# Kernel tuning notes

Measured on AMD Instinct MI355X. Metric: run time of the kernel, lower is better.

## Reference

```python
import jax, jax.numpy as jnp
import numpy as np

E = 300000
N_ATOMS = 10000
C = 256
RBF = 16
NUM_TARGET = 1


def setup_inputs() -> dict:
    key = jax.random.key(0)
    ks = jax.random.split(key, 12)
    s = lambda fan_in: 1.0 / np.sqrt(fan_in)
    return {
        "x": jax.random.normal(ks[0], (E, C), dtype=jnp.float32),
        "rbf": jax.random.uniform(ks[1], (E, RBF), dtype=jnp.float32),
        "num_atoms": N_ATOMS,
        "edge_index_0": jax.random.randint(ks[2], (E,), 0, N_ATOMS, dtype=jnp.int64),
        # lin_rbf: Linear(rbf_dim -> in_channels)
        "w_rbf": jax.random.normal(ks[3], (C, RBF), dtype=jnp.float32) * s(RBF),
        "b_rbf": jnp.zeros((C,), dtype=jnp.float32),
        # mlp: Linear(C,C), SiLU, Linear(C,C), SiLU, Linear(C, num_target)
        "w1": jax.random.normal(ks[4], (C, C), dtype=jnp.float32) * s(C),
        "b1": jnp.zeros((C,), dtype=jnp.float32),
        "w2": jax.random.normal(ks[5], (C, C), dtype=jnp.float32) * s(C),
        "b2": jnp.zeros((C,), dtype=jnp.float32),
        "w3": jax.random.normal(ks[6], (NUM_TARGET, C), dtype=jnp.float32) * s(C),
        "b3": jnp.zeros((NUM_TARGET,), dtype=jnp.float32),
    }


def reference(x, rbf, num_atoms, edge_index_0, w_rbf, b_rbf, w1, b1, w2, b2, w3, b3):
    # rbf_filter = lin_rbf(rbf): [E, C]
    rbf_filter = rbf @ w_rbf.T + b_rbf
    msg = rbf_filter * x  # [E, C]
    # scatter_add over edge source -> per-atom features [num_atoms, C]
    out = jax.ops.segment_sum(msg, edge_index_0, num_segments=num_atoms)
    # MLP: Linear+SiLU, Linear+SiLU, Linear
    out = jax.nn.silu(out @ w1.T + b1)
    out = jax.nn.silu(out @ w2.T + b2)
    out = out @ w3.T + b3  # [num_atoms, num_target]
    return out
```

## Files before the change

kernel.cpp:

```cpp
#include <hip/hip_runtime.h>
#include <math.h>

#define CDIM 256
#define RBFD 16
#define NATOMS 10000

__device__ __forceinline__ float dot4f(float4 a, float4 b) {
  return a.x * b.x + a.y * b.y + a.z * b.z + a.w * b.w;
}

__global__ void hist_kernel(const int* __restrict__ eidx, int* __restrict__ counts,
                            int E) {
  const int i = blockIdx.x * blockDim.x + threadIdx.x;
  if (i < E) atomicAdd(&counts[eidx[i]], 1);
}

__global__ void scan_kernel(const int* __restrict__ counts,
                            int* __restrict__ offsets, int* __restrict__ cursor) {
  __shared__ int part[256];
  const int t = threadIdx.x;
  const int CH = (NATOMS + 255) / 256;
  const int base = t * CH;
  const int n = min(CH, max(0, NATOMS - base));
  int s = 0;
  for (int j = 0; j < n; ++j) s += counts[base + j];
  part[t] = s;
  __syncthreads();
  for (int off = 1; off < 256; off <<= 1) {
    int v = 0;
    if (t >= off) v = part[t - off];
    __syncthreads();
    part[t] += v;
    __syncthreads();
  }
  int run = part[t] - s;
  for (int j = 0; j < n; ++j) {
    offsets[base + j] = run;
    cursor[base + j] = run;
    run += counts[base + j];
  }
  if (t == 255) offsets[NATOMS] = part[255];
}

__global__ void scatter_kernel(const int* __restrict__ eidx,
                               int* __restrict__ cursor, int* __restrict__ elist,
                               int E) {
  const int i = blockIdx.x * blockDim.x + threadIdx.x;
  if (i < E) {
    const int a = eidx[i];
    const int pos = atomicAdd(&cursor[a], 1);
    elist[pos] = i;
  }
}

__global__ __launch_bounds__(256) void gather_kernel(
    const float* __restrict__ x, const float* __restrict__ rbf,
    const int* __restrict__ elist, const int* __restrict__ offsets,
    const float* __restrict__ w_rbf, const float* __restrict__ b_rbf,
    float* __restrict__ acc) {
  const int lane = threadIdx.x & 63;
  const int atom = (blockIdx.x * blockDim.x + threadIdx.x) >> 6;
  if (atom >= NATOMS) return;
  const int c0 = lane * 4;

  const int start = offsets[atom];
  const int end = offsets[atom + 1];

  float4 wv[4][4];
  const float4 bb = *(const float4*)(b_rbf + c0);
#pragma unroll
  for (int j = 0; j < 4; ++j) {
    const float4* wr = (const float4*)(w_rbf + (size_t)(c0 + j) * RBFD);
    wv[j][0] = wr[0];
    wv[j][1] = wr[1];
    wv[j][2] = wr[2];
    wv[j][3] = wr[3];
  }

  if (end <= start) {
    *(float4*)(acc + (size_t)atom * CDIM + c0) = make_float4(0.f, 0.f, 0.f, 0.f);
    return;
  }
  const int last = end - 1;

  float4 sumA = make_float4(0.f, 0.f, 0.f, 0.f);
  float4 sumB = make_float4(0.f, 0.f, 0.f, 0.f);
  float4 sumC = make_float4(0.f, 0.f, 0.f, 0.f);

  float4 xA, xB, xC;
  float4 rA0, rA1, rA2, rA3;
  float4 rB0, rB1, rB2, rB3;
  float4 rC0, rC1, rC2, rC3;

#define LOADD(S, idv)                                                        \
  {                                                                          \
    const int e_ = __builtin_amdgcn_readfirstlane(idv);                      \
    x##S = *(const float4*)(x + (size_t)e_ * CDIM + c0);                     \
    const float4* q_ = (const float4*)(rbf + (size_t)e_ * RBFD);             \
    r##S##0 = q_[0];                                                         \
    r##S##1 = q_[1];                                                         \
    r##S##2 = q_[2];                                                         \
    r##S##3 = q_[3];                                                         \
  }

#define COMPUTE(S, sum)                                                      \
  {                                                                          \
    float4 f_;                                                               \
    f_.x = bb.x + dot4f(wv[0][0], r##S##0) + dot4f(wv[0][1], r##S##1) +      \
           dot4f(wv[0][2], r##S##2) + dot4f(wv[0][3], r##S##3);              \
    f_.y = bb.y + dot4f(wv[1][0], r##S##0) + dot4f(wv[1][1], r##S##1) +      \
           dot4f(wv[1][2], r##S##2) + dot4f(wv[1][3], r##S##3);              \
    f_.z = bb.z + dot4f(wv[2][0], r##S##0) + dot4f(wv[2][1], r##S##1) +      \
           dot4f(wv[2][2], r##S##2) + dot4f(wv[2][3], r##S##3);              \
    f_.w = bb.w + dot4f(wv[3][0], r##S##0) + dot4f(wv[3][1], r##S##1) +      \
           dot4f(wv[3][2], r##S##2) + dot4f(wv[3][3], r##S##3);              \
    sum.x += f_.x * x##S.x;                                                  \
    sum.y += f_.y * x##S.y;                                                  \
    sum.z += f_.z * x##S.z;                                                  \
    sum.w += f_.w * x##S.w;                                                  \
  }

  int idA = elist[start];
  int idB = elist[min(start + 1, last)];
  int idC = elist[min(start + 2, last)];
  LOADD(A, idA)
  LOADD(B, idB)

  int i = start;
  for (; i + 3 <= end; i += 3) {
    idA = elist[min(i + 3, last)];
    LOADD(C, idC)
    COMPUTE(A, sumA)
    idB = elist[min(i + 4, last)];
    LOADD(A, idA)
    COMPUTE(B, sumB)
    idC = elist[min(i + 5, last)];
    LOADD(B, idB)
    COMPUTE(C, sumC)
  }
  const int k = end - i;
  if (k >= 1) COMPUTE(A, sumA)
  if (k >= 2) COMPUTE(B, sumB)

#undef LOADD
#undef COMPUTE

  float4 sum;
  sum.x = sumA.x + sumB.x + sumC.x;
  sum.y = sumA.y + sumB.y + sumC.y;
  sum.z = sumA.z + sumB.z + sumC.z;
  sum.w = sumA.w + sumB.w + sumC.w;
  *(float4*)(acc + (size_t)atom * CDIM + c0) = sum;
}

__global__ void transpose_kernel(const float* __restrict__ w1,
                                 const float* __restrict__ w2,
                                 float* __restrict__ w1T,
                                 float* __restrict__ w2T) {
  __shared__ float tile[32][33];
  const float* src = blockIdx.z ? w2 : w1;
  float* dst = blockIdx.z ? w2T : w1T;
  const int bx = blockIdx.x * 32;
  const int by = blockIdx.y * 32;
  const int tx = threadIdx.x, ty = threadIdx.y;
#pragma unroll
  for (int i = 0; i < 32; i += 8)
    tile[ty + i][tx] = src[(size_t)(by + ty + i) * CDIM + bx + tx];
  __syncthreads();
#pragma unroll
  for (int i = 0; i < 32; i += 8)
    dst[(size_t)(bx + ty + i) * CDIM + by + tx] = tile[tx][ty + i];
}

__global__ __launch_bounds__(256, 2) void mlp_kernel(
    const float* __restrict__ hin, const float* __restrict__ w1T,
    const float* __restrict__ b1, const float* __restrict__ w2T,
    const float* __restrict__ b2, const float* __restrict__ w3,
    const float* __restrict__ b3, float* __restrict__ out, int natoms) {
  __shared__ float H[32 * 256];
  __shared__ float WK[32 * 256];
  const int tid = threadIdx.x;
  const int tc = tid & 31;
  const int ta = tid >> 5;
  const int a0 = blockIdx.x * 32;
  const int cA = tc * 4;
  const int cB = 128 + tc * 4;

  {
    const float4* src = (const float4*)hin + (size_t)a0 * 64;
    float4* Hv = (float4*)H;
#pragma unroll
    for (int i = 0; i < 8; ++i) {
      const int idx = tid + i * 256;
      const int ga = a0 + (idx >> 6);
      Hv[idx] = (ga < natoms) ? src[idx] : make_float4(0.f, 0.f, 0.f, 0.f);
    }
  }

  float s[4][8];

#pragma unroll 1
  for (int layer = 0; layer < 2; ++layer) {
    const float* wT = (layer == 0) ? w1T : w2T;
    const float* bias = (layer == 0) ? b1 : b2;
    float r[4][8];
    const float4 bA = *(const float4*)(bias + cA);
    const float4 bB = *(const float4*)(bias + cB);
#pragma unroll
    for (int a = 0; a < 4; ++a) {
      r[a][0] = bA.x; r[a][1] = bA.y; r[a][2] = bA.z; r[a][3] = bA.w;
      r[a][4] = bB.x; r[a][5] = bB.y; r[a][6] = bB.z; r[a][7] = bB.w;
    }

    for (int k0 = 0; k0 < 256; k0 += 32) {
      __syncthreads();
      {
        const float4* wsrc = (const float4*)(wT + (size_t)k0 * CDIM);
        float4* WKv = (float4*)WK;
#pragma unroll
        for (int i = 0; i < 8; ++i) WKv[tid + i * 256] = wsrc[tid + i * 256];
      }
      __syncthreads();

#pragma unroll
      for (int kk = 0; kk < 32; kk += 4) {
        float4 ha[4];
#pragma unroll
        for (int a = 0; a < 4; ++a)
          ha[a] = *(const float4*)&H[(ta * 4 + a) * 256 + k0 + kk];
#pragma unroll
        for (int u = 0; u < 4; ++u) {
          const float4 w0 = *(const float4*)&WK[(kk + u) * 256 + cA];
          const float4 w1v = *(const float4*)&WK[(kk + u) * 256 + cB];
#pragma unroll
          for (int a = 0; a < 4; ++a) {
            const float hv = (u == 0) ? ha[a].x
                           : (u == 1) ? ha[a].y
                           : (u == 2) ? ha[a].z : ha[a].w;
            r[a][0] += hv * w0.x;  r[a][1] += hv * w0.y;
            r[a][2] += hv * w0.z;  r[a][3] += hv * w0.w;
            r[a][4] += hv * w1v.x; r[a][5] += hv * w1v.y;
            r[a][6] += hv * w1v.z; r[a][7] += hv * w1v.w;
          }
        }
      }
    }

#pragma unroll
    for (int a = 0; a < 4; ++a)
#pragma unroll
      for (int j = 0; j < 8; ++j) {
        const float v = r[a][j];
        s[a][j] = v / (1.0f + __expf(-v));
      }

    if (layer == 0) {
      __syncthreads();
#pragma unroll
      for (int a = 0; a < 4; ++a) {
        *(float4*)&H[(ta * 4 + a) * 256 + cA] =
            make_float4(s[a][0], s[a][1], s[a][2], s[a][3]);
        *(float4*)&H[(ta * 4 + a) * 256 + cB] =
            make_float4(s[a][4], s[a][5], s[a][6], s[a][7]);
      }
    }
  }

  const float4 w3a = *(const float4*)(w3 + cA);
  const float4 w3b = *(const float4*)(w3 + cB);
  float part[4];
#pragma unroll
  for (int a = 0; a < 4; ++a) {
    part[a] = s[a][0] * w3a.x + s[a][1] * w3a.y + s[a][2] * w3a.z +
              s[a][3] * w3a.w + s[a][4] * w3b.x + s[a][5] * w3b.y +
              s[a][6] * w3b.z + s[a][7] * w3b.w;
  }
  __syncthreads();
  float* red = WK;
#pragma unroll
  for (int a = 0; a < 4; ++a) red[(ta * 4 + a) * 33 + tc] = part[a];
  __syncthreads();
  if (tid < 32) {
    float sum = 0.f;
#pragma unroll
    for (int j = 0; j < 32; ++j) sum += red[tid * 33 + j];
    const int ga = a0 + tid;
    if (ga < natoms) out[ga] = sum + b3[0];
  }
}

extern "C" void kernel_launch(void* const* d_in, const int* in_sizes, int n_in,
                              void* d_out, int out_size, void* d_ws,
                              size_t ws_size, hipStream_t stream) {
  const float* x = (const float*)d_in[0];
  const float* rbf = (const float*)d_in[1];
  const int* eidx = (const int*)d_in[3];
  const float* w_rbf = (const float*)d_in[4];
  const float* b_rbf = (const float*)d_in[5];
  const float* w1 = (const float*)d_in[6];
  const float* b1 = (const float*)d_in[7];
  const float* w2 = (const float*)d_in[8];
  const float* b2 = (const float*)d_in[9];
  const float* w3 = (const float*)d_in[10];
  const float* b3 = (const float*)d_in[11];
  float* out = (float*)d_out;
  const int E = in_sizes[0] / CDIM;

  char* p = (char*)d_ws;
  float* acc = (float*)p;              p += (size_t)NATOMS * CDIM * sizeof(float);
  float* w1T = (float*)p;              p += CDIM * CDIM * sizeof(float);
  float* w2T = (float*)p;              p += CDIM * CDIM * sizeof(float);
  int* counts = (int*)p;               p += NATOMS * sizeof(int);
  int* offsets = (int*)p;              p += (NATOMS + 1) * sizeof(int);
  int* cursor = (int*)p;               p += NATOMS * sizeof(int);
  int* elist = (int*)p;                p += (size_t)E * sizeof(int);

  hipMemsetAsync(counts, 0, NATOMS * sizeof(int), stream);
  hist_kernel<<<(E + 255) / 256, 256, 0, stream>>>(eidx, counts, E);
  scan_kernel<<<1, 256, 0, stream>>>(counts, offsets, cursor);
  scatter_kernel<<<(E + 255) / 256, 256, 0, stream>>>(eidx, cursor, elist, E);
  transpose_kernel<<<dim3(8, 8, 2), dim3(32, 8), 0, stream>>>(w1, w2, w1T, w2T);
  gather_kernel<<<(NATOMS * 64 + 255) / 256, 256, 0, stream>>>(
      x, rbf, elist, offsets, w_rbf, b_rbf, acc);
  mlp_kernel<<<(NATOMS + 31) / 32, 256, 0, stream>>>(acc, w1T, b1, w2T, b2, w3,
                                                     b3, out, NATOMS);
}
```

Measured before the change: 629.9 us.

## Use one block per atom with one channel per thread in gather

The gather kernel now assigns a whole 256-thread block to each atom, with each thread owning a single channel, where before one wavefront per atom had each lane handle four channels. Each thread keeps only 16 filter weights in registers instead of 64, and launch bounds ask for 5 blocks per CU to raise occupancy and latency hiding. The cost is that four wavefronts now each re-read the same elist entries and rbf rows, and x is loaded as scalar floats rather than float4 vectors.

Measured after the change: 627.1 us. About the same (-0.5%).

```diff
diff --git a/kernel.cpp b/kernel.cpp
--- a/kernel.cpp
+++ b/kernel.cpp
@@ -5,7 +5,7 @@
 #define RBFD 16
 #define NATOMS 10000
 
-__device__ __forceinline__ float dot4f(float4 a, float4 b) {
+__device__ __forceinline__ float dot44(float4 a, float4 b) {
   return a.x * b.x + a.y * b.y + a.z * b.z + a.w * b.w;
 }
 
@@ -53,50 +53,47 @@
   }
 }
 
-__global__ __launch_bounds__(256) void gather_kernel(
+__global__ __launch_bounds__(256, 5) void gather_kernel(
     const float* __restrict__ x, const float* __restrict__ rbf,
     const int* __restrict__ elist, const int* __restrict__ offsets,
     const float* __restrict__ w_rbf, const float* __restrict__ b_rbf,
     float* __restrict__ acc) {
-  const int lane = threadIdx.x & 63;
-  const int atom = (blockIdx.x * blockDim.x + threadIdx.x) >> 6;
-  if (atom >= NATOMS) return;
-  const int c0 = lane * 4;
-
-  const int start = offsets[atom];
-  const int end = offsets[atom + 1];
-
-  float4 wv[4][4];
-  const float4 bb = *(const float4*)(b_rbf + c0);
-#pragma unroll
-  for (int j = 0; j < 4; ++j) {
-    const float4* wr = (const float4*)(w_rbf + (size_t)(c0 + j) * RBFD);
-    wv[j][0] = wr[0];
-    wv[j][1] = wr[1];
-    wv[j][2] = wr[2];
-    wv[j][3] = wr[3];
-  }
+  const int tid = threadIdx.x;
+  const int lane = tid & 63;
+  const int w = tid >> 6;
+  const int atom = blockIdx.x;
+  const int ch = w * 64 + lane;
+
+  const int start = __builtin_amdgcn_readfirstlane(offsets[atom]);
+  const int end = __builtin_amdgcn_readfirstlane(offsets[atom + 1]);
+
+  float4 wv0, wv1, wv2, wv3;
+  {
+    const float4* wr = (const float4*)(w_rbf + (size_t)ch * RBFD);
+    wv0 = wr[0];
+    wv1 = wr[1];
+    wv2 = wr[2];
+    wv3 = wr[3];
+  }
+  const float bb = b_rbf[ch];
 
   if (end <= start) {
-    *(float4*)(acc + (size_t)atom * CDIM + c0) = make_float4(0.f, 0.f, 0.f, 0.f);
+    acc[(size_t)atom * CDIM + ch] = 0.f;
     return;
   }
   const int last = end - 1;
 
-  float4 sumA = make_float4(0.f, 0.f, 0.f, 0.f);
-  float4 sumB = make_float4(0.f, 0.f, 0.f, 0.f);
-  float4 sumC = make_float4(0.f, 0.f, 0.f, 0.f);
-
-  float4 xA, xB, xC;
+  float sumA = 0.f, sumB = 0.f, sumC = 0.f;
+
+  float xA, xB, xC;
   float4 rA0, rA1, rA2, rA3;
   float4 rB0, rB1, rB2, rB3;
   float4 rC0, rC1, rC2, rC3;
 
-#define LOADD(S, idv)                                                        \
+#define LOADD(S, eid)                                                        \
   {                                                                          \
-    const int e_ = __builtin_amdgcn_readfirstlane(idv);                      \
-    x##S = *(const float4*)(x + (size_t)e_ * CDIM + c0);                     \
-    const float4* q_ = (const float4*)(rbf + (size_t)e_ * RBFD);             \
+    x##S = x[(size_t)(eid)*CDIM + ch];           \
+    const float4* q_ = (const float4*)(rbf + (size_t)(eid)*RBFD);            \
     r##S##0 = q_[0];                                                         \
     r##S##1 = q_[1];                                                         \
     r##S##2 = q_[2];                                                         \
@@ -105,36 +102,26 @@
 
 #define COMPUTE(S, sum)                                                      \
   {                                                                          \
-    float4 f_;                                                               \
-    f_.x = bb.x + dot4f(wv[0][0], r##S##0) + dot4f(wv[0][1], r##S##1) +      \
-           dot4f(wv[0][2], r##S##2) + dot4f(wv[0][3], r##S##3);              \
-    f_.y = bb.y + dot4f(wv[1][0], r##S##0) + dot4f(wv[1][1], r##S##1) +      \
-           dot4f(wv[1][2], r##S##2) + dot4f(wv[1][3], r##S##3);              \
-    f_.z = bb.z + dot4f(wv[2][0], r##S##0) + dot4f(wv[2][1], r##S##1) +      \
-           dot4f(wv[2][2], r##S##2) + dot4f(wv[2][3], r##S##3);              \
-    f_.w = bb.w + dot4f(wv[3][0], r##S##0) + dot4f(wv[3][1], r##S##1) +      \
-           dot4f(wv[3][2], r##S##2) + dot4f(wv[3][3], r##S##3);              \
-    sum.x += f_.x * x##S.x;                                                  \
-    sum.y += f_.y * x##S.y;                                                  \
-    sum.z += f_.z * x##S.z;                                                  \
-    sum.w += f_.w * x##S.w;                                                  \
-  }
-
-  int idA = elist[start];
-  int idB = elist[min(start + 1, last)];
-  int idC = elist[min(start + 2, last)];
+    const float f_ = bb + dot44(wv0, r##S##0) + dot44(wv1, r##S##1) +        \
+                     dot44(wv2, r##S##2) + dot44(wv3, r##S##3);              \
+    sum += f_ * x##S;                                                        \
+  }
+
+  int idA = __builtin_amdgcn_readfirstlane(elist[start]);
+  int idB = __builtin_amdgcn_readfirstlane(elist[min(start + 1, last)]);
+  int idC = __builtin_amdgcn_readfirstlane(elist[min(start + 2, last)]);
   LOADD(A, idA)
   LOADD(B, idB)
 
   int i = start;
   for (; i + 3 <= end; i += 3) {
-    idA = elist[min(i + 3, last)];
+    idA = __builtin_amdgcn_readfirstlane(elist[min(i + 3, last)]);
     LOADD(C, idC)
     COMPUTE(A, sumA)
-    idB = elist[min(i + 4, last)];
+    idB = __builtin_amdgcn_readfirstlane(elist[min(i + 4, last)]);
     LOADD(A, idA)
     COMPUTE(B, sumB)
-    idC = elist[min(i + 5, last)];
+    idC = __builtin_amdgcn_readfirstlane(elist[min(i + 5, last)]);
     LOADD(B, idB)
     COMPUTE(C, sumC)
   }
@@ -145,12 +132,7 @@
 #undef LOADD
 #undef COMPUTE
 
-  float4 sum;
-  sum.x = sumA.x + sumB.x + sumC.x;
-  sum.y = sumA.y + sumB.y + sumC.y;
-  sum.z = sumA.z + sumB.z + sumC.z;
-  sum.w = sumA.w + sumB.w + sumC.w;
-  *(float4*)(acc + (size_t)atom * CDIM + c0) = sum;
+  acc[(size_t)atom * CDIM + ch] = sumA + sumB + sumC;
 }
 
 __global__ void transpose_kernel(const float* __restrict__ w1,
@@ -320,8 +302,8 @@
   scan_kernel<<<1, 256, 0, stream>>>(counts, offsets, cursor);
   scatter_kernel<<<(E + 255) / 256, 256, 0, stream>>>(eidx, cursor, elist, E);
   transpose_kernel<<<dim3(8, 8, 2), dim3(32, 8), 0, stream>>>(w1, w2, w1T, w2T);
-  gather_kernel<<<(NATOMS * 64 + 255) / 256, 256, 0, stream>>>(
-      x, rbf, elist, offsets, w_rbf, b_rbf, acc);
+  gather_kernel<<<NATOMS, 256, 0, stream>>>(x, rbf, elist, offsets, w_rbf,
+                                            b_rbf, acc);
   mlp_kernel<<<(NATOMS + 31) / 32, 256, 0, stream>>>(acc, w1T, b1, w2T, b2, w3,
                                                      b3, out, NATOMS);
 }
```
